# Kernel tuning notes

Hardware: AMD Instinct MI355X
Metric: run time of the kernel (lower is better)

## Reference

```python
import jax, jax.numpy as jnp
import numpy as np

D = 128      # input_dim (= out_channels = edge_dim)
H = 2        # n_head
N_ENT = 100000
B = 64       # number of queries / batches
R = 500      # number of relations
E = 400000   # number of original edges
NEG = 0.2    # GATv2 leaky_relu negative slope


def setup_inputs() -> dict:
    key = jax.random.key(0)
    ks = jax.random.split(key, 10)
    s = 1.0 / np.sqrt(D)
    queries = jax.random.normal(ks[0], (B, D), jnp.float32)
    entities = jax.random.normal(ks[1], (N_ENT, D), jnp.float32)
    edge_index = jax.random.randint(ks[2], (2, E), 0, N_ENT)
    relations = jax.random.normal(ks[3], (R, D), jnp.float32)
    relation_index = jax.random.randint(ks[4], (E,), 0, R)
    # guarantees batch.max()+1 == queries.shape[0] (module assert)
    batch = jnp.arange(N_ENT, dtype=jnp.int32) % B
    # GATv2Conv params: lin_l / lin_r (bias=True), lin_edge (bias=False), att, bias
    W_l = jax.random.normal(ks[5], (H * D, D), jnp.float32) * s
    b_l = jnp.zeros((H * D,), jnp.float32)
    W_r = jax.random.normal(ks[6], (H * D, D), jnp.float32) * s
    b_r = jnp.zeros((H * D,), jnp.float32)
    W_ea = jax.random.normal(ks[7], (H * D, D), jnp.float32) * s
    att = jax.random.normal(ks[8], (H, D), jnp.float32) * s
    bias = jnp.zeros((D,), jnp.float32)  # concat=False -> size out_channels
    # outer Injector.lin_edge: Linear(H*D, D, bias=True)
    W_le = jax.random.normal(ks[9], (D, H * D), jnp.float32) / np.sqrt(H * D)
    b_le = jnp.zeros((D,), jnp.float32)
    return dict(queries=queries, entities=entities, edge_index=edge_index,
                relations=relations, relation_index=relation_index, batch=batch,
                W_l=W_l, b_l=b_l, W_r=W_r, b_r=b_r, W_ea=W_ea, att=att,
                bias=bias, W_le=W_le, b_le=b_le)


def reference(queries, entities, edge_index, relations, relation_index, batch,
              W_l, b_l, W_r, b_r, W_ea, att, bias, W_le, b_le):
    n_ent = entities.shape[0]
    node = jnp.vstack([entities, queries])                        # [N+B, D]
    rel_feat = jnp.vstack([relations,
                           jnp.ones((1, relations.shape[1]), relations.dtype)])
    # added edges: query -> its entities
    src = jnp.concatenate([edge_index[0], batch.astype(edge_index.dtype) + n_ent])
    tgt = jnp.concatenate([edge_index[1],
                           jnp.arange(n_ent, dtype=edge_index.dtype)])
    rel_idx = jnp.concatenate([relation_index,
                               jnp.full((n_ent,), rel_feat.shape[0] - 1,
                                        relation_index.dtype)])
    edge_attr = rel_feat[rel_idx]                                  # [Etot, D]

    n_tot = node.shape[0]
    x_l = (node @ W_l.T + b_l).reshape(n_tot, H, D)                # source proj
    x_r = (node @ W_r.T + b_r).reshape(n_tot, H, D)                # target proj
    e = (edge_attr @ W_ea.T).reshape(-1, H, D)                     # [Etot, H, D]

    xj = x_l[src]                                                  # gather per edge
    z = jax.nn.leaky_relu(xj + x_r[tgt] + e, NEG)                  # [Etot, H, D]
    alpha = jnp.einsum('ehd,hd->eh', z, att)                       # [Etot, H]
    # segment softmax over target nodes
    amax = jax.ops.segment_max(alpha, tgt, num_segments=n_tot)
    alpha = jnp.exp(alpha - amax[tgt])
    denom = jax.ops.segment_sum(alpha, tgt, num_segments=n_tot)
    alpha = alpha / (denom[tgt] + 1e-16)

    msg = xj * alpha[..., None]                                    # [Etot, H, D]
    agg = jax.ops.segment_sum(msg, tgt, num_segments=n_tot)        # [Ntot, H, D]
    out = agg.mean(axis=1) + bias                                  # concat=False
    out_node = out[:n_ent]

    out_edge = jax.nn.relu(relations @ W_ea.T)                     # [R, H*D]
    out_edge = out_edge @ W_le.T + b_le                            # [R, D]
    return (out_node, out_edge)
```

## Files before the change

### kernel.cpp

```cpp
#include <hip/hip_runtime.h>
#include <math.h>

#define D 128
#define HD 256
#define N_ENT 100000
#define NBATCH 64
#define NTOT (N_ENT + NBATCH)
#define RCOUNT 500
#define E_BASE 400000
#define ETOT (E_BASE + N_ENT)
#define NEG 0.2f
#define SCAN_NB 391
#define CPAD (SCAN_NB * 256)

#define WCAST_NB 64
#define ZERO_NB SCAN_NB
#define REL_NB (RCOUNT + 1)
#define PREP_NB (WCAST_NB + ZERO_NB + REL_NB)

#define GEMM_NB ((NTOT + 63) / 64)
#define HIST_NB ((ETOT + 255) / 256)

typedef __attribute__((ext_vector_type(8))) short bf16x8;
typedef __attribute__((ext_vector_type(8))) unsigned short u16x8;
typedef __attribute__((ext_vector_type(4))) float f32x4;

static __device__ __forceinline__ unsigned short f2bf(float f) {
  unsigned u = __builtin_bit_cast(unsigned, f);
  u += 0x7fffu + ((u >> 16) & 1u);
  return (unsigned short)(u >> 16);
}
static __device__ __forceinline__ float bf2f(unsigned short h) {
  return __builtin_bit_cast(float, (unsigned)h << 16);
}

__global__ __launch_bounds__(256) void k_prep(
    const float* __restrict__ W_l, const float* __restrict__ W_r,
    unsigned short* __restrict__ Wbf,
    const float* __restrict__ relations, const float* __restrict__ W_ea,
    const float* __restrict__ W_le, const float* __restrict__ b_le,
    unsigned short* __restrict__ e_rel, float* __restrict__ out_edge,
    int* __restrict__ counts) {
  __shared__ float relu_p[HD];
  int bx = blockIdx.x;
  int tid = threadIdx.x;
  if (bx < WCAST_NB) {
    int e4 = (bx * 256 + tid) * 4;
    int v = e4 >> 7;
    int k = e4 & 127;
    const float* src = (v < HD) ? (W_l + (size_t)v * D + k) : (W_r + (size_t)(v - HD) * D + k);
    float4 a = *(const float4*)src;
    *(ushort4*)(Wbf + (size_t)v * D + k) = make_ushort4(f2bf(a.x), f2bf(a.y), f2bf(a.z), f2bf(a.w));
    return;
  }
  if (bx < WCAST_NB + ZERO_NB) {
    counts[(bx - WCAST_NB) * 256 + tid] = 0;
    return;
  }
  int r = bx - (WCAST_NB + ZERO_NB);
  int j = tid;
  const float* w = W_ea + (size_t)j * D;
  float acc = 0.f;
  if (r < RCOUNT) {
    const float* rel = relations + (size_t)r * D;
    for (int k = 0; k < D; k += 4) {
      float4 a = *(const float4*)(rel + k);
      float4 b = *(const float4*)(w + k);
      acc += a.x * b.x + a.y * b.y + a.z * b.z + a.w * b.w;
    }
  } else {
    for (int k = 0; k < D; k += 4) {
      float4 b = *(const float4*)(w + k);
      acc += b.x + b.y + b.z + b.w;
    }
  }
  e_rel[(size_t)r * HD + j] = f2bf(acc);
  if (r < RCOUNT) {
    relu_p[j] = acc > 0.f ? acc : 0.f;
    __syncthreads();
    if (j < D) {
      const float* wl = W_le + (size_t)j * HD;
      float o = b_le[j];
      for (int k = 0; k < HD; k += 4) {
        float4 p4 = *(const float4*)(relu_p + k);
        float4 w4 = *(const float4*)(wl + k);
        o += p4.x * w4.x + p4.y * w4.y + p4.z * w4.z + p4.w * w4.w;
      }
      out_edge[(size_t)r * D + j] = o;
    }
  }
}

#define LDA 136

__global__ __launch_bounds__(256) void k_gemm_mfma(
    const float* __restrict__ entities, const float* __restrict__ queries,
    const unsigned short* __restrict__ Wbf,
    const float* __restrict__ b_l, const float* __restrict__ b_r,
    unsigned short* __restrict__ x_l, unsigned short* __restrict__ x_r,
    const int* __restrict__ edge_index, int* __restrict__ counts) {
  __shared__ unsigned short As[64 * LDA];
  __shared__ unsigned short Cs[64 * LDA];
  int tid = threadIdx.x;
  if (blockIdx.x >= GEMM_NB) {
    int e = (blockIdx.x - GEMM_NB) * 256 + tid;
    if (e < ETOT) {
      int t = (e < E_BASE) ? edge_index[E_BASE + e] : (e - E_BASE);
      atomicAdd(counts + t, 1);
    }
    return;
  }
  int rb = blockIdx.x;

  {
    int rr = tid >> 2;
    int part = (tid & 3) * 32;
    int row = rb * 64 + rr;
    const float* sp;
    if (row < N_ENT) sp = entities + (size_t)row * D;
    else if (row < NTOT) sp = queries + (size_t)(row - N_ENT) * D;
    else sp = entities;
#pragma unroll
    for (int k = 0; k < 32; k += 8) {
      float4 a0 = *(const float4*)(sp + part + k);
      float4 a1 = *(const float4*)(sp + part + k + 4);
      u16x8 p;
      p[0] = f2bf(a0.x); p[1] = f2bf(a0.y); p[2] = f2bf(a0.z); p[3] = f2bf(a0.w);
      p[4] = f2bf(a1.x); p[5] = f2bf(a1.y); p[6] = f2bf(a1.z); p[7] = f2bf(a1.w);
      *(u16x8*)(&As[rr * LDA + part + k]) = p;
    }
  }
  __syncthreads();

  int w = tid >> 6, lane = tid & 63;
  int wr = w >> 1, wc = w & 1;
  int m = lane & 15, q8 = (lane >> 4) * 8;

  for (int ccv = 0; ccv < 4; ccv++) {
    bool isL = ccv < 2;
    const float* bv = isL ? b_l : b_r;
    unsigned short* xdst = isL ? x_l : x_r;
    int cbase = (ccv & 1) * 128;

    f32x4 acc[2][4];
#pragma unroll
    for (int i = 0; i < 2; i++)
#pragma unroll
      for (int j = 0; j < 4; j++) acc[i][j] = (f32x4){0.f, 0.f, 0.f, 0.f};

    const unsigned short* wbase = Wbf + (size_t)(ccv * 128 + wc * 64 + m) * D;
#pragma unroll
    for (int ks = 0; ks < 128; ks += 32) {
      bf16x8 af[2], bfr[4];
#pragma unroll
      for (int i = 0; i < 2; i++)
        af[i] = *(const bf16x8*)(&As[(wr * 32 + i * 16 + m) * LDA + ks + q8]);
#pragma unroll
      for (int j = 0; j < 4; j++)
        bfr[j] = *(const bf16x8*)(wbase + (size_t)j * 16 * D + ks + q8);
#pragma unroll
      for (int i = 0; i < 2; i++)
#pragma unroll
        for (int j = 0; j < 4; j++)
          acc[i][j] = __builtin_amdgcn_mfma_f32_16x16x32_bf16(af[i], bfr[j], acc[i][j], 0, 0, 0);
    }

    __syncthreads();
#pragma unroll
    for (int j = 0; j < 4; j++) {
      int col = wc * 64 + j * 16 + m;
      float bb = bv[cbase + col];
#pragma unroll
      for (int i = 0; i < 2; i++) {
        int row0 = wr * 32 + i * 16 + (lane >> 4) * 4;
#pragma unroll
        for (int r = 0; r < 4; r++)
          Cs[(row0 + r) * LDA + col] = f2bf(acc[i][j][r] + bb);
      }
    }
    __syncthreads();
#pragma unroll
    for (int it = 0; it < 4; it++) {
      int g = it * 256 + tid;
      int row = g >> 4, c8 = (g & 15) * 8;
      int grow = rb * 64 + row;
      if (grow < NTOT) {
        u16x8 v = *(const u16x8*)(&Cs[row * LDA + c8]);
        *(u16x8*)(xdst + (size_t)grow * HD + cbase + c8) = v;
      }
    }
  }
}

__global__ __launch_bounds__(256) void k_scan_a(const int* __restrict__ counts, int* __restrict__ bsum) {
  __shared__ int sd[256];
  int tid = threadIdx.x;
  sd[tid] = counts[blockIdx.x * 256 + tid];
  __syncthreads();
  for (int off = 128; off > 0; off >>= 1) {
    if (tid < off) sd[tid] += sd[tid + off];
    __syncthreads();
  }
  if (tid == 0) bsum[blockIdx.x] = sd[0];
}

__global__ __launch_bounds__(256) void k_scan_b(
    const int* __restrict__ counts, const int* __restrict__ bsum,
    int* __restrict__ offsets, int* __restrict__ cursor) {
  __shared__ int s[256];
  int b = blockIdx.x, tid = threadIdx.x;
  int part = 0;
  if (tid < b) part += bsum[tid];
  if (tid + 256 < b) part += bsum[tid + 256];
  s[tid] = part;
  __syncthreads();
  for (int off = 128; off > 0; off >>= 1) {
    if (tid < off) s[tid] += s[tid + off];
    __syncthreads();
  }
  int pre_sum = s[0];
  __syncthreads();
  int v = counts[b * 256 + tid];
  s[tid] = v;
  __syncthreads();
  for (int off = 1; off < 256; off <<= 1) {
    int y = (tid >= off) ? s[tid - off] : 0;
    __syncthreads();
    s[tid] += y;
    __syncthreads();
  }
  int excl = pre_sum + s[tid] - v;
  int i = b * 256 + tid;
  if (i <= N_ENT) offsets[i] = excl;
  if (i < N_ENT) cursor[i] = excl;
}

__global__ void k_scatter(const int* __restrict__ edge_index, const int* __restrict__ relation_index,
                          const int* __restrict__ batch, int* __restrict__ cursor,
                          unsigned int* __restrict__ sorted) {
  int e = blockIdx.x * 256 + threadIdx.x;
  if (e >= ETOT) return;
  int s, t, r;
  if (e < E_BASE) {
    s = edge_index[e];
    t = edge_index[E_BASE + e];
    r = relation_index[e];
  } else {
    int i = e - E_BASE;
    s = N_ENT + batch[i];
    t = i;
    r = RCOUNT;
  }
  int pos = atomicAdd(cursor + t, 1);
  sorted[pos] = (unsigned)s | ((unsigned)r << 17);
}

__global__ __launch_bounds__(256) void k_edge(
    const unsigned short* __restrict__ x_l, const unsigned short* __restrict__ x_r,
    const unsigned short* __restrict__ e_rel, const int* __restrict__ offsets,
    const unsigned int* __restrict__ sorted, const float* __restrict__ att,
    const float* __restrict__ bias, float* __restrict__ out) {
  int wv = threadIdx.x >> 6;
  int lane = threadIdx.x & 63;
  int t = blockIdx.x * 4 + wv;
  int half = lane >> 5;
  int sl = lane & 31;
  int elem = sl * 8;
  u16x8 xr8 = *(const u16x8*)(x_r + (size_t)t * HD + elem);
  float xr[8], at[8];
#pragma unroll
  for (int i = 0; i < 8; i++) xr[i] = bf2f(xr8[i]);
  float4 at0 = *(const float4*)(att + elem);
  float4 at1 = *(const float4*)(att + elem + 4);
  at[0] = at0.x; at[1] = at0.y; at[2] = at0.z; at[3] = at0.w;
  at[4] = at1.x; at[5] = at1.y; at[6] = at1.z; at[7] = at1.w;
  int e0 = offsets[t], e1 = offsets[t + 1];
  float denom = 0.f;
  float acc[8];
#pragma unroll
  for (int i = 0; i < 8; i++) acc[i] = 0.f;

  int e = e0;
  for (; e + 4 <= e1; e += 4) {
    unsigned srA = sorted[e + half];
    unsigned srB = sorted[e + 2 + half];
    const unsigned short* pA = x_l + (size_t)(srA & 0x1FFFF) * HD + elem;
    const unsigned short* qA = e_rel + (size_t)(srA >> 17) * HD + elem;
    const unsigned short* pB = x_l + (size_t)(srB & 0x1FFFF) * HD + elem;
    const unsigned short* qB = e_rel + (size_t)(srB >> 17) * HD + elem;
    u16x8 xlA = *(const u16x8*)pA;
    u16x8 erA = *(const u16x8*)qA;
    u16x8 xlB = *(const u16x8*)pB;
    u16x8 erB = *(const u16x8*)qB;
    float xa[8], xb[8];
    float pa = 0.f, pb = 0.f;
#pragma unroll
    for (int i = 0; i < 8; i++) {
      xa[i] = bf2f(xlA[i]);
      float za = xa[i] + xr[i] + bf2f(erA[i]);
      za = za > 0.f ? za : NEG * za;
      pa += za * at[i];
      xb[i] = bf2f(xlB[i]);
      float zb = xb[i] + xr[i] + bf2f(erB[i]);
      zb = zb > 0.f ? zb : NEG * zb;
      pb += zb * at[i];
    }
    pa += __shfl_xor(pa, 1, 64);  pb += __shfl_xor(pb, 1, 64);
    pa += __shfl_xor(pa, 2, 64);  pb += __shfl_xor(pb, 2, 64);
    pa += __shfl_xor(pa, 4, 64);  pb += __shfl_xor(pb, 4, 64);
    pa += __shfl_xor(pa, 8, 64);  pb += __shfl_xor(pb, 8, 64);
    float wa = __expf(pa);
    float wb = __expf(pb);
    denom += wa + wb;
#pragma unroll
    for (int i = 0; i < 8; i++) acc[i] += wa * xa[i] + wb * xb[i];
  }
  for (; e < e1; e += 2) {
    int ee = e + half;
    bool valid = ee < e1;
    unsigned sr = sorted[valid ? ee : e0];
    int s = sr & 0x1FFFF;
    int r = sr >> 17;
    u16x8 xl8 = *(const u16x8*)(x_l + (size_t)s * HD + elem);
    u16x8 er8 = *(const u16x8*)(e_rel + (size_t)r * HD + elem);
    float xl[8];
    float p = 0.f;
#pragma unroll
    for (int i = 0; i < 8; i++) {
      xl[i] = bf2f(xl8[i]);
      float z = xl[i] + xr[i] + bf2f(er8[i]);
      z = z > 0.f ? z : NEG * z;
      p += z * at[i];
    }
    p += __shfl_xor(p, 1, 64);
    p += __shfl_xor(p, 2, 64);
    p += __shfl_xor(p, 4, 64);
    p += __shfl_xor(p, 8, 64);
    float wgt = valid ? __expf(p) : 0.f;
    denom += wgt;
#pragma unroll
    for (int i = 0; i < 8; i++) acc[i] += wgt * xl[i];
  }
  denom += __shfl_xor(denom, 32, 64);
#pragma unroll
  for (int i = 0; i < 8; i++) acc[i] += __shfl_xor(acc[i], 32, 64);
  float inv = 1.f / (denom + 1e-16f);
  float o[8];
#pragma unroll
  for (int i = 0; i < 8; i++) o[i] = acc[i] * inv;
#pragma unroll
  for (int i = 0; i < 8; i++) o[i] += __shfl_xor(o[i], 16, 64);
  if (lane < 16) {
    int d = sl * 8;
    float4 b0 = *(const float4*)(bias + d);
    float4 b1 = *(const float4*)(bias + d + 4);
    *(float4*)(out + (size_t)t * D + d) =
        make_float4(o[0] * 0.5f + b0.x, o[1] * 0.5f + b0.y, o[2] * 0.5f + b0.z, o[3] * 0.5f + b0.w);
    *(float4*)(out + (size_t)t * D + d + 4) =
        make_float4(o[4] * 0.5f + b1.x, o[5] * 0.5f + b1.y, o[6] * 0.5f + b1.z, o[7] * 0.5f + b1.w);
  }
}

extern "C" void kernel_launch(void* const* d_in, const int* in_sizes, int n_in,
                              void* d_out, int out_size, void* d_ws, size_t ws_size,
                              hipStream_t stream) {
  const float* queries = (const float*)d_in[0];
  const float* entities = (const float*)d_in[1];
  const int* edge_index = (const int*)d_in[2];
  const float* relations = (const float*)d_in[3];
  const int* relation_index = (const int*)d_in[4];
  const int* batch = (const int*)d_in[5];
  const float* W_l = (const float*)d_in[6];
  const float* b_l = (const float*)d_in[7];
  const float* W_r = (const float*)d_in[8];
  const float* b_r = (const float*)d_in[9];
  const float* W_ea = (const float*)d_in[10];
  const float* att = (const float*)d_in[11];
  const float* bias = (const float*)d_in[12];
  const float* W_le = (const float*)d_in[13];
  const float* b_le = (const float*)d_in[14];

  float* out_node = (float*)d_out;
  float* out_edge = out_node + (size_t)N_ENT * D;

  char* base = (char*)d_ws;
  size_t off = 0;
  auto take = [&](size_t nbytes) -> void* {
    void* p = base + off;
    off += (nbytes + 255) & ~(size_t)255;
    return p;
  };
  unsigned short* x_l = (unsigned short*)take((size_t)NTOT * HD * sizeof(unsigned short));
  unsigned short* x_r = (unsigned short*)take((size_t)NTOT * HD * sizeof(unsigned short));
  unsigned short* e_rel = (unsigned short*)take((size_t)(RCOUNT + 1) * HD * sizeof(unsigned short));
  unsigned short* Wbf = (unsigned short*)take((size_t)512 * D * sizeof(unsigned short));
  int* counts = (int*)take((size_t)CPAD * sizeof(int));
  int* offsets = (int*)take((size_t)(N_ENT + 1) * sizeof(int));
  int* cursor = (int*)take((size_t)N_ENT * sizeof(int));
  int* bsum = (int*)take(512 * sizeof(int));
  unsigned int* sorted = (unsigned int*)take((size_t)ETOT * sizeof(unsigned int));

  k_prep<<<dim3(PREP_NB), dim3(256), 0, stream>>>(W_l, W_r, Wbf, relations, W_ea, W_le, b_le,
                                                  e_rel, out_edge, counts);
  k_gemm_mfma<<<dim3(GEMM_NB + HIST_NB), dim3(256), 0, stream>>>(entities, queries, Wbf, b_l, b_r,
                                                                 x_l, x_r, edge_index, counts);
  k_scan_a<<<dim3(SCAN_NB), dim3(256), 0, stream>>>(counts, bsum);
  k_scan_b<<<dim3(SCAN_NB), dim3(256), 0, stream>>>(counts, bsum, offsets, cursor);
  k_scatter<<<dim3(HIST_NB), dim3(256), 0, stream>>>(edge_index, relation_index, batch, cursor, sorted);
  k_edge<<<dim3(N_ENT / 4), dim3(256), 0, stream>>>(x_l, x_r, e_rel, offsets, sorted, att, bias, out_node);
}
```

Before: 305.0 us.

## Coarsen edge kernel to four targets per wave with packed math and byte offsets

Each wavefront in the edge-aggregation kernel now handles four consecutive target nodes instead of one, so the grid shrinks by four. The next target's x_r row is prefetched while the current one is processed. The scatter stage stores precomputed byte offsets for source and relation rows as a uint2 pair, which removes the per-edge mask and multiply but doubles the size of the sorted edge array. The per-edge attention math now uses packed two-wide float ops, the 0.5 head-mean factor is folded into the softmax normalizer, and output stores and x_r loads are nontemporal.

```diff
diff --git a/kernel.cpp b/kernel.cpp
--- a/kernel.cpp
+++ b/kernel.cpp
@@ -20,10 +20,12 @@
 
 #define GEMM_NB ((NTOT + 63) / 64)
 #define HIST_NB ((ETOT + 255) / 256)
+#define EDGE_NB 6250
 
 typedef __attribute__((ext_vector_type(8))) short bf16x8;
 typedef __attribute__((ext_vector_type(8))) unsigned short u16x8;
 typedef __attribute__((ext_vector_type(4))) float f32x4;
+typedef __attribute__((ext_vector_type(2))) float f32x2;
 
 static __device__ __forceinline__ unsigned short f2bf(float f) {
   unsigned u = __builtin_bit_cast(unsigned, f);
@@ -32,6 +34,12 @@
 }
 static __device__ __forceinline__ float bf2f(unsigned short h) {
   return __builtin_bit_cast(float, (unsigned)h << 16);
+}
+static __device__ __forceinline__ f32x2 bfpair(unsigned u) {
+  f32x2 r;
+  r[0] = __builtin_bit_cast(float, u << 16);
+  r[1] = __builtin_bit_cast(float, u & 0xffff0000u);
+  return r;
 }
 
 __global__ __launch_bounds__(256) void k_prep(
@@ -237,7 +245,7 @@
 
 __global__ void k_scatter(const int* __restrict__ edge_index, const int* __restrict__ relation_index,
                           const int* __restrict__ batch, int* __restrict__ cursor,
-                          unsigned int* __restrict__ sorted) {
+                          uint2* __restrict__ sorted) {
   int e = blockIdx.x * 256 + threadIdx.x;
   if (e >= ETOT) return;
   int s, t, r;
@@ -252,112 +260,141 @@
     r = RCOUNT;
   }
   int pos = atomicAdd(cursor + t, 1);
-  sorted[pos] = (unsigned)s | ((unsigned)r << 17);
+  sorted[pos] = make_uint2((unsigned)s << 9, (unsigned)r << 9);
+}
+
+static __device__ __forceinline__ float edge_accum(
+    u16x8 xl8, u16x8 er8, const f32x2* __restrict__ xr2,
+    const f32x2* __restrict__ at2, f32x2* __restrict__ x2) {
+  uint4 xu = __builtin_bit_cast(uint4, xl8);
+  uint4 eu = __builtin_bit_cast(uint4, er8);
+  unsigned xw[4] = {xu.x, xu.y, xu.z, xu.w};
+  unsigned ew[4] = {eu.x, eu.y, eu.z, eu.w};
+  f32x2 p2 = (f32x2){0.f, 0.f};
+#pragma unroll
+  for (int i = 0; i < 4; ++i) {
+    f32x2 x = bfpair(xw[i]);
+    x2[i] = x;
+    f32x2 z = (x + xr2[i]) + bfpair(ew[i]);
+    f32x2 zn = z * NEG;
+    z[0] = fmaxf(z[0], zn[0]);
+    z[1] = fmaxf(z[1], zn[1]);
+    p2 += z * at2[i];
+  }
+  return p2[0] + p2[1];
 }
 
 __global__ __launch_bounds__(256) void k_edge(
     const unsigned short* __restrict__ x_l, const unsigned short* __restrict__ x_r,
     const unsigned short* __restrict__ e_rel, const int* __restrict__ offsets,
-    const unsigned int* __restrict__ sorted, const float* __restrict__ att,
+    const uint2* __restrict__ sorted, const float* __restrict__ att,
     const float* __restrict__ bias, float* __restrict__ out) {
   int wv = threadIdx.x >> 6;
   int lane = threadIdx.x & 63;
-  int t = blockIdx.x * 4 + wv;
   int half = lane >> 5;
   int sl = lane & 31;
   int elem = sl * 8;
-  u16x8 xr8 = *(const u16x8*)(x_r + (size_t)t * HD + elem);
-  float xr[8], at[8];
-#pragma unroll
-  for (int i = 0; i < 8; i++) xr[i] = bf2f(xr8[i]);
-  float4 at0 = *(const float4*)(att + elem);
-  float4 at1 = *(const float4*)(att + elem + 4);
-  at[0] = at0.x; at[1] = at0.y; at[2] = at0.z; at[3] = at0.w;
-  at[4] = at1.x; at[5] = at1.y; at[6] = at1.z; at[7] = at1.w;
-  int e0 = offsets[t], e1 = offsets[t + 1];
-  float denom = 0.f;
-  float acc[8];
-#pragma unroll
-  for (int i = 0; i < 8; i++) acc[i] = 0.f;
-
-  int e = e0;
-  for (; e + 4 <= e1; e += 4) {
-    unsigned srA = sorted[e + half];
-    unsigned srB = sorted[e + 2 + half];
-    const unsigned short* pA = x_l + (size_t)(srA & 0x1FFFF) * HD + elem;
-    const unsigned short* qA = e_rel + (size_t)(srA >> 17) * HD + elem;
-    const unsigned short* pB = x_l + (size_t)(srB & 0x1FFFF) * HD + elem;
-    const unsigned short* qB = e_rel + (size_t)(srB >> 17) * HD + elem;
-    u16x8 xlA = *(const u16x8*)pA;
-    u16x8 erA = *(const u16x8*)qA;
-    u16x8 xlB = *(const u16x8*)pB;
-    u16x8 erB = *(const u16x8*)qB;
-    float xa[8], xb[8];
-    float pa = 0.f, pb = 0.f;
-#pragma unroll
-    for (int i = 0; i < 8; i++) {
-      xa[i] = bf2f(xlA[i]);
-      float za = xa[i] + xr[i] + bf2f(erA[i]);
-      za = za > 0.f ? za : NEG * za;
-      pa += za * at[i];
-      xb[i] = bf2f(xlB[i]);
-      float zb = xb[i] + xr[i] + bf2f(erB[i]);
-      zb = zb > 0.f ? zb : NEG * zb;
-      pb += zb * at[i];
-    }
-    pa += __shfl_xor(pa, 1, 64);  pb += __shfl_xor(pb, 1, 64);
-    pa += __shfl_xor(pa, 2, 64);  pb += __shfl_xor(pb, 2, 64);
-    pa += __shfl_xor(pa, 4, 64);  pb += __shfl_xor(pb, 4, 64);
-    pa += __shfl_xor(pa, 8, 64);  pb += __shfl_xor(pb, 8, 64);
-    float wa = __expf(pa);
-    float wb = __expf(pb);
-    denom += wa + wb;
-#pragma unroll
-    for (int i = 0; i < 8; i++) acc[i] += wa * xa[i] + wb * xb[i];
-  }
-  for (; e < e1; e += 2) {
-    int ee = e + half;
-    bool valid = ee < e1;
-    unsigned sr = sorted[valid ? ee : e0];
-    int s = sr & 0x1FFFF;
-    int r = sr >> 17;
-    u16x8 xl8 = *(const u16x8*)(x_l + (size_t)s * HD + elem);
-    u16x8 er8 = *(const u16x8*)(e_rel + (size_t)r * HD + elem);
-    float xl[8];
-    float p = 0.f;
-#pragma unroll
-    for (int i = 0; i < 8; i++) {
-      xl[i] = bf2f(xl8[i]);
-      float z = xl[i] + xr[i] + bf2f(er8[i]);
-      z = z > 0.f ? z : NEG * z;
-      p += z * at[i];
-    }
-    p += __shfl_xor(p, 1, 64);
-    p += __shfl_xor(p, 2, 64);
-    p += __shfl_xor(p, 4, 64);
-    p += __shfl_xor(p, 8, 64);
-    float wgt = valid ? __expf(p) : 0.f;
-    denom += wgt;
-#pragma unroll
-    for (int i = 0; i < 8; i++) acc[i] += wgt * xl[i];
-  }
-  denom += __shfl_xor(denom, 32, 64);
-#pragma unroll
-  for (int i = 0; i < 8; i++) acc[i] += __shfl_xor(acc[i], 32, 64);
-  float inv = 1.f / (denom + 1e-16f);
-  float o[8];
-#pragma unroll
-  for (int i = 0; i < 8; i++) o[i] = acc[i] * inv;
-#pragma unroll
-  for (int i = 0; i < 8; i++) o[i] += __shfl_xor(o[i], 16, 64);
-  if (lane < 16) {
-    int d = sl * 8;
-    float4 b0 = *(const float4*)(bias + d);
-    float4 b1 = *(const float4*)(bias + d + 4);
-    *(float4*)(out + (size_t)t * D + d) =
-        make_float4(o[0] * 0.5f + b0.x, o[1] * 0.5f + b0.y, o[2] * 0.5f + b0.z, o[3] * 0.5f + b0.w);
-    *(float4*)(out + (size_t)t * D + d + 4) =
-        make_float4(o[4] * 0.5f + b1.x, o[5] * 0.5f + b1.y, o[6] * 0.5f + b1.z, o[7] * 0.5f + b1.w);
+  int t0 = (blockIdx.x * 4 + wv) * 4;
+
+  const char* xlb = (const char*)x_l + elem * 2;
+  const char* erb = (const char*)e_rel + elem * 2;
+
+  f32x2 at2[4];
+  {
+    float4 a0 = *(const float4*)(att + elem);
+    float4 a1 = *(const float4*)(att + elem + 4);
+    at2[0] = (f32x2){a0.x, a0.y};
+    at2[1] = (f32x2){a0.z, a0.w};
+    at2[2] = (f32x2){a1.x, a1.y};
+    at2[3] = (f32x2){a1.z, a1.w};
+  }
+  int4 ofs = *(const int4*)(offsets + t0);
+  int eb[5];
+  eb[0] = ofs.x; eb[1] = ofs.y; eb[2] = ofs.z; eb[3] = ofs.w;
+  eb[4] = offsets[t0 + 4];
+
+  u16x8 xr8 = __builtin_nontemporal_load((const u16x8*)(x_r + (size_t)t0 * HD + elem));
+
+#pragma unroll
+  for (int ti = 0; ti < 4; ++ti) {
+    f32x2 xr2[4];
+    {
+      uint4 u = __builtin_bit_cast(uint4, xr8);
+      xr2[0] = bfpair(u.x); xr2[1] = bfpair(u.y);
+      xr2[2] = bfpair(u.z); xr2[3] = bfpair(u.w);
+    }
+    xr8 = __builtin_nontemporal_load((const u16x8*)(x_r + (size_t)(t0 + ti + 1) * HD + elem));
+
+    int e0 = eb[ti], e1 = eb[ti + 1];
+    f32x2 acc2[4];
+    acc2[0] = acc2[1] = acc2[2] = acc2[3] = (f32x2){0.f, 0.f};
+    float denom = 0.f;
+    int e = e0;
+    for (; e + 4 <= e1; e += 4) {
+      uint2 srA = sorted[e + half];
+      uint2 srB = sorted[e + 2 + half];
+      u16x8 xlA = *(const u16x8*)(xlb + srA.x);
+      u16x8 erA = *(const u16x8*)(erb + srA.y);
+      u16x8 xlB = *(const u16x8*)(xlb + srB.x);
+      u16x8 erB = *(const u16x8*)(erb + srB.y);
+      f32x2 xa2[4], xb2[4];
+      float pa = edge_accum(xlA, erA, xr2, at2, xa2);
+      float pb = edge_accum(xlB, erB, xr2, at2, xb2);
+      pa += __shfl_xor(pa, 1, 64);  pb += __shfl_xor(pb, 1, 64);
+      pa += __shfl_xor(pa, 2, 64);  pb += __shfl_xor(pb, 2, 64);
+      pa += __shfl_xor(pa, 4, 64);  pb += __shfl_xor(pb, 4, 64);
+      pa += __shfl_xor(pa, 8, 64);  pb += __shfl_xor(pb, 8, 64);
+      float wa = __expf(pa);
+      float wb = __expf(pb);
+      denom += wa + wb;
+#pragma unroll
+      for (int i = 0; i < 4; ++i) {
+        acc2[i] += xa2[i] * wa;
+        acc2[i] += xb2[i] * wb;
+      }
+    }
+    for (; e < e1; e += 2) {
+      int ee = e + half;
+      bool valid = ee < e1;
+      uint2 sr = sorted[valid ? ee : e0];
+      u16x8 xl8 = *(const u16x8*)(xlb + sr.x);
+      u16x8 er8 = *(const u16x8*)(erb + sr.y);
+      f32x2 x2[4];
+      float p = edge_accum(xl8, er8, xr2, at2, x2);
+      p += __shfl_xor(p, 1, 64);
+      p += __shfl_xor(p, 2, 64);
+      p += __shfl_xor(p, 4, 64);
+      p += __shfl_xor(p, 8, 64);
+      float wgt = valid ? __expf(p) : 0.f;
+      denom += wgt;
+#pragma unroll
+      for (int i = 0; i < 4; ++i) acc2[i] += x2[i] * wgt;
+    }
+    denom += __shfl_xor(denom, 32, 64);
+#pragma unroll
+    for (int i = 0; i < 4; ++i) {
+      acc2[i][0] += __shfl_xor(acc2[i][0], 32, 64);
+      acc2[i][1] += __shfl_xor(acc2[i][1], 32, 64);
+    }
+    float inv = 0.5f / (denom + 1e-16f);
+    float o[8];
+#pragma unroll
+    for (int i = 0; i < 4; ++i) {
+      o[2 * i] = acc2[i][0] * inv;
+      o[2 * i + 1] = acc2[i][1] * inv;
+    }
+#pragma unroll
+    for (int i = 0; i < 8; ++i) o[i] += __shfl_xor(o[i], 16, 64);
+    if (lane < 16) {
+      int t = t0 + ti;
+      int d = sl * 8;
+      float4 b0 = *(const float4*)(bias + d);
+      float4 b1 = *(const float4*)(bias + d + 4);
+      f32x4 s0 = (f32x4){o[0] + b0.x, o[1] + b0.y, o[2] + b0.z, o[3] + b0.w};
+      f32x4 s1 = (f32x4){o[4] + b1.x, o[5] + b1.y, o[6] + b1.z, o[7] + b1.w};
+      __builtin_nontemporal_store(s0, (f32x4*)(out + (size_t)t * D + d));
+      __builtin_nontemporal_store(s1, (f32x4*)(out + (size_t)t * D + d + 4));
+    }
   }
 }
 
@@ -398,7 +435,7 @@
   int* offsets = (int*)take((size_t)(N_ENT + 1) * sizeof(int));
   int* cursor = (int*)take((size_t)N_ENT * sizeof(int));
   int* bsum = (int*)take(512 * sizeof(int));
-  unsigned int* sorted = (unsigned int*)take((size_t)ETOT * sizeof(unsigned int));
+  uint2* sorted = (uint2*)take((size_t)ETOT * sizeof(uint2));
 
   k_prep<<<dim3(PREP_NB), dim3(256), 0, stream>>>(W_l, W_r, Wbf, relations, W_ea, W_le, b_le,
                                                   e_rel, out_edge, counts);
@@ -407,5 +444,5 @@
   k_scan_a<<<dim3(SCAN_NB), dim3(256), 0, stream>>>(counts, bsum);
   k_scan_b<<<dim3(SCAN_NB), dim3(256), 0, stream>>>(counts, bsum, offsets, cursor);
   k_scatter<<<dim3(HIST_NB), dim3(256), 0, stream>>>(edge_index, relation_index, batch, cursor, sorted);
-  k_edge<<<dim3(N_ENT / 4), dim3(256), 0, stream>>>(x_l, x_r, e_rel, offsets, sorted, att, bias, out_node);
-}
+  k_edge<<<dim3(EDGE_NB), dim3(256), 0, stream>>>(x_l, x_r, e_rel, offsets, sorted, att, bias, out_node);
+}
```

Result: no change. 303.2 us (-0.6%).
